# Performance work log

Measured on AMD Instinct MI355X. Metric: run time of the kernel, lower is better.

The kernel has to match this reference:

```python
import jax, jax.numpy as jnp
import numpy as np

N_NODES = 50000


def _gcn_conv(h, W, b, src, dst, dinv):
    # PyG GCNConv: linear transform, then symmetric-normalized sum aggregation
    h = h @ W  # (N, d_out)
    norm = dinv[src] * dinv[dst]  # (E,)
    msg = h[src] * norm[:, None]  # (E, d_out)
    agg = jax.ops.segment_sum(msg, dst, num_segments=N_NODES)
    return agg + b


def setup_inputs() -> dict:
    key = jax.random.key(0)
    ks = jax.random.split(key, 9)
    in_dim, h1, h2, out_dim = 512, 512, 512, 256
    x = jax.random.normal(ks[0], (N_NODES, in_dim), dtype=jnp.float32)
    edge_index = jax.random.randint(ks[1], (2, 800000), 0, N_NODES, dtype=jnp.int64)

    def glorot(k, shape):
        lim = float(np.sqrt(6.0 / (shape[0] + shape[1])))
        return jax.random.uniform(k, shape, jnp.float32, -lim, lim)

    return {
        "x": x,
        "edge_index": edge_index,
        "W1": glorot(ks[2], (in_dim, h1)),
        "b1": jnp.zeros((h1,), jnp.float32),
        "W2": glorot(ks[3], (h1, h2)),
        "b2": jnp.zeros((h2,), jnp.float32),
        "Wout": glorot(ks[4], (h2, out_dim)),
        "bout": jnp.zeros((out_dim,), jnp.float32),
    }


def reference(x, edge_index, W1, b1, W2, b2, Wout, bout):
    # add self-loops (GCNConv default)
    loop = jnp.arange(N_NODES, dtype=edge_index.dtype)
    src = jnp.concatenate([edge_index[0], loop])
    dst = jnp.concatenate([edge_index[1], loop])
    # degree on A + I (target side), deg^{-1/2}
    deg = jax.ops.segment_sum(jnp.ones_like(dst, dtype=x.dtype), dst, num_segments=N_NODES)
    dinv = jnp.where(deg > 0, jax.lax.rsqrt(deg), 0.0)

    h = jax.nn.relu(_gcn_conv(x, W1, b1, src, dst, dinv))
    h = jax.nn.relu(_gcn_conv(h, W2, b2, src, dst, dinv))
    return h @ Wout + bout
```

## Files before the change

kernel.cpp:

```cpp
#include <hip/hip_runtime.h>

#define NN 50000
#define MP 50048
#define DD 512
#define EE 800000
#define NSCAN 196
#define SCB 3321
#define CNTB 3125
#define WTB 2560
#define CVB 25024
#define CSRTOT (EE + NN + 3 * NN + 64)

typedef unsigned short u16;
typedef __attribute__((ext_vector_type(4))) float f32x4;
typedef __attribute__((ext_vector_type(8))) __bf16 bf16x8;
typedef __attribute__((ext_vector_type(8))) short s16x8;
typedef __attribute__((ext_vector_type(4))) short s16x4;

typedef __attribute__((address_space(1))) const void GVoid;
typedef __attribute__((address_space(3))) void LVoid;

__device__ __forceinline__ u16 f2bf(float f) {
  union { float f; unsigned u; } x; x.f = f;
  unsigned r = x.u + 0x7fffu + ((x.u >> 16) & 1u);
  return (u16)(r >> 16);
}
__device__ __forceinline__ float bf2f(u16 b) {
  union { unsigned u; float f; } x; x.u = ((unsigned)b) << 16;
  return x.f;
}


__global__ __launch_bounds__(256) void prep_k(const int* __restrict__ dst, int* __restrict__ cnt,
                                              const float* __restrict__ W1, u16* __restrict__ W1T,
                                              const float* __restrict__ W2, u16* __restrict__ W2T,
                                              const float* __restrict__ Wo, u16* __restrict__ WoT,
                                              const float* __restrict__ x, u16* __restrict__ xb) {
  const int b = (int)blockIdx.x, t = threadIdx.x;
  if (b < CNTB) {
    int e = b * 256 + t;
    atomicAdd(&cnt[dst[e]], 1);
    return;
  }
  if (b < CNTB + WTB) {
    int b0 = b - CNTB;
    const float* W; u16* WT; int idx, k, n;
    if (b0 < 1024)      { W = W1; WT = W1T; idx = b0 * 256 + t;          k = idx >> 9; n = idx & 511; WT[n * 512 + k] = f2bf(W[idx]); }
    else if (b0 < 2048) { W = W2; WT = W2T; idx = (b0 - 1024) * 256 + t; k = idx >> 9; n = idx & 511; WT[n * 512 + k] = f2bf(W[idx]); }
    else                { W = Wo; WT = WoT; idx = (b0 - 2048) * 256 + t; k = idx >> 8; n = idx & 255; WT[n * 512 + k] = f2bf(W[idx]); }
    return;
  }
  size_t i = ((size_t)(b - CNTB - WTB) * 256 + t) * 4;
  if (i >= (size_t)MP * DD) return;
  s16x4 v;
  if (i < (size_t)NN * DD) {
    f32x4 f = *(const f32x4*)(x + i);
    v = (s16x4){ (short)f2bf(f.x), (short)f2bf(f.y), (short)f2bf(f.z), (short)f2bf(f.w) };
  } else {
    v = (s16x4){ 0, 0, 0, 0 };
  }
  *(s16x4*)(xb + i) = v;
}


__global__ __launch_bounds__(256) void scan1_k(const int* __restrict__ cnt, int* __restrict__ bsum) {
  __shared__ int s[256];
  const int t = threadIdx.x;
  const int i = blockIdx.x * 256 + t;
  s[t] = (i < NN) ? ((cnt[i] + 1 + 3) & ~3) : 0;
  __syncthreads();
  for (int off = 128; off > 0; off >>= 1) {
    if (t < off) s[t] += s[t + off];
    __syncthreads();
  }
  if (t == 0) bsum[blockIdx.x] = s[0];
}

__global__ __launch_bounds__(256) void scan2_k(const int* __restrict__ bsum, int* __restrict__ boff) {
  __shared__ int s[256];
  const int t = threadIdx.x;
  const int v = (t < NSCAN) ? bsum[t] : 0;
  s[t] = v;
  __syncthreads();
  for (int off = 1; off < 256; off <<= 1) {
    int a = s[t];
    int b = (t >= off) ? s[t - off] : 0;
    __syncthreads();
    s[t] = a + b;
    __syncthreads();
  }
  if (t < NSCAN) boff[t] = s[t] - v;
}

__global__ __launch_bounds__(256) void scan3_k(const int* __restrict__ cnt, const int* __restrict__ boff,
                                               int* __restrict__ rowp, int* __restrict__ cursor,
                                               float* __restrict__ dinv) {
  __shared__ int s[256];
  const int t = threadIdx.x;
  const int i = blockIdx.x * 256 + t;
  const int v = (i < NN) ? (cnt[i] + 1) : 0;
  const int pv = (v + 3) & ~3;
  s[t] = pv;
  __syncthreads();
  for (int off = 1; off < 256; off <<= 1) {
    int a = s[t];
    int b = (t >= off) ? s[t - off] : 0;
    __syncthreads();
    s[t] = a + b;
    __syncthreads();
  }
  const int excl = s[t] - pv + boff[blockIdx.x];
  if (i < NN) {
    rowp[i] = excl; cursor[i] = excl;
    dinv[i] = rsqrtf((float)v);
  }
  if (i == NN - 1) rowp[NN] = excl + pv;
}


__global__ __launch_bounds__(256) void scatter_k(const int* __restrict__ src, const int* __restrict__ dst,
                                                 const float* __restrict__ dinv, int* __restrict__ cursor,
                                                 int2* __restrict__ csr) {
  int e = (int)blockIdx.x * 256 + threadIdx.x;
  if (e < EE) {
    int d = dst[e], sn = src[e];
    int pos = atomicAdd(&cursor[d], 1);
    csr[pos] = make_int2(sn << 10, __float_as_int(dinv[sn] * dinv[d]));
  } else if (e < EE + NN) {
    int i = e - EE;
    int pos = atomicAdd(&cursor[i], 1);
    float di = dinv[i];
    csr[pos] = make_int2(i << 10, __float_as_int(di * di));
  }
}


template<int OUT_BF16>
__global__ __launch_bounds__(256) void gemm_k(const u16* __restrict__ A, const u16* __restrict__ BT,
                                              void* __restrict__ Cv, const float* __restrict__ bias,
                                              int M, int N) {
  const int nwg = (int)gridDim.x;
  const int id = (int)blockIdx.x;
  const int xcd = id & 7;
  const int idx = id >> 3;
  const int q = nwg >> 3, r = nwg & 7;
  const int tile = (xcd < r ? xcd * (q + 1) : r * (q + 1) + (xcd - r) * q) + idx;
  const int ntn = N >> 7;
  const int bm = tile / ntn;
  const int bn = tile % ntn;

  __shared__ u16 As[2][128 * 32];
  __shared__ u16 Bs[2][128 * 32];
  const int t = threadIdx.x;
  const int lane = t & 63;
  const int wc = (t >> 6) & 1;
  const int wr = (t >> 7) & 1;
  f32x4 acc[4][4] = {};
  const int r0 = t >> 2;
  const int kc = (t & 3) * 8;
  const u16* Ab = A + (size_t)bm * 128 * DD + (size_t)r0 * DD + kc;
  const u16* Bb = BT + (size_t)bn * 128 * DD + (size_t)r0 * DD + kc;

  auto stage = [&](int buf, int kt) {
    __builtin_amdgcn_global_load_lds((GVoid*)(Ab + kt),           (LVoid*)(&As[buf][t * 8]),        16, 0, 0);
    __builtin_amdgcn_global_load_lds((GVoid*)(Ab + 64 * DD + kt), (LVoid*)(&As[buf][2048 + t * 8]), 16, 0, 0);
    __builtin_amdgcn_global_load_lds((GVoid*)(Bb + kt),           (LVoid*)(&Bs[buf][t * 8]),        16, 0, 0);
    __builtin_amdgcn_global_load_lds((GVoid*)(Bb + 64 * DD + kt), (LVoid*)(&Bs[buf][2048 + t * 8]), 16, 0, 0);
  };

  stage(0, 0);
  __syncthreads();

  #pragma unroll 2
  for (int step = 0; step < 16; ++step) {
    const int cur = step & 1;
    if (step < 15) stage(cur ^ 1, (step + 1) * 32);
    bf16x8 af[4], bv[4];
    #pragma unroll
    for (int m = 0; m < 4; ++m)
      af[m] = *(const bf16x8*)&As[cur][(wr * 64 + m * 16 + (lane & 15)) * 32 + (lane >> 4) * 8];
    #pragma unroll
    for (int n = 0; n < 4; ++n)
      bv[n] = *(const bf16x8*)&Bs[cur][(wc * 64 + n * 16 + (lane & 15)) * 32 + (lane >> 4) * 8];
    #pragma unroll
    for (int m = 0; m < 4; ++m) {
      #pragma unroll
      for (int n = 0; n < 4; ++n)
        acc[m][n] = __builtin_amdgcn_mfma_f32_16x16x32_bf16(af[m], bv[n], acc[m][n], 0, 0, 0);
    }
    __syncthreads();
  }

  const int rb = bm * 128 + wr * 64 + ((lane >> 4) * 4);
  const int cb = bn * 128 + wc * 64 + (lane & 15);
  #pragma unroll
  for (int m = 0; m < 4; ++m) {
    #pragma unroll
    for (int rr = 0; rr < 4; ++rr) {
      const int row = rb + m * 16 + rr;
      if (row < M) {
        #pragma unroll
        for (int n = 0; n < 4; ++n) {
          const int col = cb + n * 16;
          float v = acc[m][n][rr];
          if (bias) v += bias[col];
          if (OUT_BF16) ((u16*)Cv)[(size_t)row * N + col] = f2bf(v);
          else          ((float*)Cv)[(size_t)row * N + col] = v;
        }
      }
    }
  }
}


__global__ __launch_bounds__(256) void aggregate_k(const u16* __restrict__ H, const int* __restrict__ rowp,
                                                   const int2* __restrict__ csr,
                                                   const float* __restrict__ bias,
                                                   u16* __restrict__ out) {
  const int slice = (int)blockIdx.x & 7;
  const int grp = (int)blockIdx.x >> 3;
  const int wid = threadIdx.x >> 6;
  const int lane = threadIdx.x & 63;
  const int g = lane >> 3;
  const int l = lane & 7;
  const int node = grp * 32 + wid * 8 + g;
  if (node >= NN) return;
  const int d0 = slice * 64 + l * 8;
  const int beg = rowp[node];
  const int rounds = (rowp[node + 1] - beg) >> 2;
  const char* Hb = (const char*)H + (size_t)d0 * 2;
  const int4* cp = (const int4*)(csr + beg);
  float a0 = 0.f, a1 = 0.f, a2 = 0.f, a3 = 0.f, a4 = 0.f, a5 = 0.f, a6 = 0.f, a7 = 0.f;

  int4 c01 = cp[0], c23 = cp[1];
  for (int b = 0; b < rounds; ++b) {
    const s16x8 v0 = *(const s16x8*)(Hb + c01.x);
    const s16x8 v1 = *(const s16x8*)(Hb + c01.z);
    const s16x8 v2 = *(const s16x8*)(Hb + c23.x);
    const s16x8 v3 = *(const s16x8*)(Hb + c23.z);
    const int4 n01 = cp[2 * b + 2], n23 = cp[2 * b + 3];
    const float w0 = __int_as_float(c01.y), w1 = __int_as_float(c01.w);
    const float w2 = __int_as_float(c23.y), w3 = __int_as_float(c23.w);
    a0 += bf2f((u16)v0[0]) * w0 + bf2f((u16)v1[0]) * w1 + bf2f((u16)v2[0]) * w2 + bf2f((u16)v3[0]) * w3;
    a1 += bf2f((u16)v0[1]) * w0 + bf2f((u16)v1[1]) * w1 + bf2f((u16)v2[1]) * w2 + bf2f((u16)v3[1]) * w3;
    a2 += bf2f((u16)v0[2]) * w0 + bf2f((u16)v1[2]) * w1 + bf2f((u16)v2[2]) * w2 + bf2f((u16)v3[2]) * w3;
    a3 += bf2f((u16)v0[3]) * w0 + bf2f((u16)v1[3]) * w1 + bf2f((u16)v2[3]) * w2 + bf2f((u16)v3[3]) * w3;
    a4 += bf2f((u16)v0[4]) * w0 + bf2f((u16)v1[4]) * w1 + bf2f((u16)v2[4]) * w2 + bf2f((u16)v3[4]) * w3;
    a5 += bf2f((u16)v0[5]) * w0 + bf2f((u16)v1[5]) * w1 + bf2f((u16)v2[5]) * w2 + bf2f((u16)v3[5]) * w3;
    a6 += bf2f((u16)v0[6]) * w0 + bf2f((u16)v1[6]) * w1 + bf2f((u16)v2[6]) * w2 + bf2f((u16)v3[6]) * w3;
    a7 += bf2f((u16)v0[7]) * w0 + bf2f((u16)v1[7]) * w1 + bf2f((u16)v2[7]) * w2 + bf2f((u16)v3[7]) * w3;
    c01 = n01; c23 = n23;
  }

  s16x8 o;
  o[0] = (short)f2bf(fmaxf(a0 + bias[d0 + 0], 0.f));
  o[1] = (short)f2bf(fmaxf(a1 + bias[d0 + 1], 0.f));
  o[2] = (short)f2bf(fmaxf(a2 + bias[d0 + 2], 0.f));
  o[3] = (short)f2bf(fmaxf(a3 + bias[d0 + 3], 0.f));
  o[4] = (short)f2bf(fmaxf(a4 + bias[d0 + 4], 0.f));
  o[5] = (short)f2bf(fmaxf(a5 + bias[d0 + 5], 0.f));
  o[6] = (short)f2bf(fmaxf(a6 + bias[d0 + 6], 0.f));
  o[7] = (short)f2bf(fmaxf(a7 + bias[d0 + 7], 0.f));
  *(s16x8*)(out + (size_t)node * DD + d0) = o;
}


extern "C" void kernel_launch(void* const* d_in, const int* in_sizes, int n_in,
                              void* d_out, int out_size, void* d_ws, size_t ws_size,
                              hipStream_t stream) {
  const float* x    = (const float*)d_in[0];
  const int*   ei   = (const int*)d_in[1];
  const float* W1   = (const float*)d_in[2];
  const float* b1   = (const float*)d_in[3];
  const float* W2   = (const float*)d_in[4];
  const float* b2   = (const float*)d_in[5];
  const float* Wout = (const float*)d_in[6];
  const float* bout = (const float*)d_in[7];
  float* out = (float*)d_out;
  (void)in_sizes; (void)n_in; (void)out_size; (void)ws_size;

  char* ws = (char*)d_ws;
  size_t off = 0;
  auto alloc = [&](size_t bytes) -> char* {
    char* p = ws + off;
    off = (off + bytes + 255) & ~(size_t)255;
    return p;
  };
  u16*   xb   = (u16*)alloc((size_t)MP * DD * 2);
  u16*   H    = (u16*)alloc((size_t)NN * DD * 2);
  u16*   W1T  = (u16*)alloc(512 * 512 * 2);
  u16*   W2T  = (u16*)alloc(512 * 512 * 2);
  u16*   WoT  = (u16*)alloc(256 * 512 * 2);
  int*   cnt  = (int*)alloc(NN * 4);
  float* dinv = (float*)alloc(NN * 4);
  int*   rowp = (int*)alloc((NN + 1) * 4);
  int*   cur  = (int*)alloc(NN * 4);
  int2*  csr  = (int2*)alloc((size_t)CSRTOT * 8);
  int*   bsum = (int*)alloc(NSCAN * 4);
  int*   boff = (int*)alloc(NSCAN * 4);

  const int* srcp = ei;
  const int* dstp = ei + EE;

  hipMemsetAsync(cnt, 0, NN * 4, stream);
  hipMemsetAsync(csr, 0, (size_t)CSRTOT * 8, stream);

  prep_k<<<CNTB + WTB + CVB, 256, 0, stream>>>(dstp, cnt, W1, W1T, W2, W2T, Wout, WoT, x, xb);
  scan1_k<<<NSCAN, 256, 0, stream>>>(cnt, bsum);
  scan2_k<<<1, 256, 0, stream>>>(bsum, boff);
  scan3_k<<<NSCAN, 256, 0, stream>>>(cnt, boff, rowp, cur, dinv);
  scatter_k<<<SCB, 256, 0, stream>>>(srcp, dstp, dinv, cur, csr);

  const int agg_grid = ((NN + 31) / 32) * 8;

  gemm_k<1><<<(MP / 128) * (512 / 128), 256, 0, stream>>>(xb, W1T, (void*)H, nullptr, NN, 512);
  aggregate_k<<<agg_grid, 256, 0, stream>>>(H, rowp, csr, b1, xb);
  gemm_k<1><<<(MP / 128) * (512 / 128), 256, 0, stream>>>(xb, W2T, (void*)H, nullptr, NN, 512);
  aggregate_k<<<agg_grid, 256, 0, stream>>>(H, rowp, csr, b2, xb);
  gemm_k<0><<<(MP / 128) * (256 / 128), 256, 0, stream>>>(xb, WoT, (void*)out, bout, NN, 256);
}
```

Before: 440.0 us.

## Use 256x128 GEMM tiles, fuse weight/x conversion into scatter, nontemporal CSR loads

The GEMM tile becomes 256x128 with 512 threads, so each block reuses the B tile across twice as many rows and the grid is halved. Padding is raised to a multiple of 256 to match. The weight transpose and x-to-bf16 conversion move out of the counting kernel and into the scatter kernel launch, leaving a lean atomic count kernel. The aggregation kernel uses nontemporal loads for CSR entries and nontemporal stores for its output to reduce cache pollution. The larger tile uses more LDS and registers per block, which may lower occupancy.

```diff
diff --git a/kernel.cpp b/kernel.cpp
--- a/kernel.cpp
+++ b/kernel.cpp
@@ -1,14 +1,14 @@
 #include <hip/hip_runtime.h>
 
 #define NN 50000
-#define MP 50048
+#define MP 50176
 #define DD 512
 #define EE 800000
 #define NSCAN 196
 #define SCB 3321
 #define CNTB 3125
 #define WTB 2560
-#define CVB 25024
+#define CVB 25088
 #define CSRTOT (EE + NN + 3 * NN + 64)
 
 typedef unsigned short u16;
@@ -16,6 +16,7 @@
 typedef __attribute__((ext_vector_type(8))) __bf16 bf16x8;
 typedef __attribute__((ext_vector_type(8))) short s16x8;
 typedef __attribute__((ext_vector_type(4))) short s16x4;
+typedef __attribute__((ext_vector_type(4))) int i32x4;
 
 typedef __attribute__((address_space(1))) const void GVoid;
 typedef __attribute__((address_space(3))) void LVoid;
@@ -31,35 +32,9 @@
 }
 
 
-__global__ __launch_bounds__(256) void prep_k(const int* __restrict__ dst, int* __restrict__ cnt,
-                                              const float* __restrict__ W1, u16* __restrict__ W1T,
-                                              const float* __restrict__ W2, u16* __restrict__ W2T,
-                                              const float* __restrict__ Wo, u16* __restrict__ WoT,
-                                              const float* __restrict__ x, u16* __restrict__ xb) {
-  const int b = (int)blockIdx.x, t = threadIdx.x;
-  if (b < CNTB) {
-    int e = b * 256 + t;
-    atomicAdd(&cnt[dst[e]], 1);
-    return;
-  }
-  if (b < CNTB + WTB) {
-    int b0 = b - CNTB;
-    const float* W; u16* WT; int idx, k, n;
-    if (b0 < 1024)      { W = W1; WT = W1T; idx = b0 * 256 + t;          k = idx >> 9; n = idx & 511; WT[n * 512 + k] = f2bf(W[idx]); }
-    else if (b0 < 2048) { W = W2; WT = W2T; idx = (b0 - 1024) * 256 + t; k = idx >> 9; n = idx & 511; WT[n * 512 + k] = f2bf(W[idx]); }
-    else                { W = Wo; WT = WoT; idx = (b0 - 2048) * 256 + t; k = idx >> 8; n = idx & 255; WT[n * 512 + k] = f2bf(W[idx]); }
-    return;
-  }
-  size_t i = ((size_t)(b - CNTB - WTB) * 256 + t) * 4;
-  if (i >= (size_t)MP * DD) return;
-  s16x4 v;
-  if (i < (size_t)NN * DD) {
-    f32x4 f = *(const f32x4*)(x + i);
-    v = (s16x4){ (short)f2bf(f.x), (short)f2bf(f.y), (short)f2bf(f.z), (short)f2bf(f.w) };
-  } else {
-    v = (s16x4){ 0, 0, 0, 0 };
-  }
-  *(s16x4*)(xb + i) = v;
+__global__ __launch_bounds__(256) void count_k(const int* __restrict__ dst, int* __restrict__ cnt) {
+  int e = (int)blockIdx.x * 256 + threadIdx.x;
+  atomicAdd(&cnt[dst[e]], 1);
 }
 
 
@@ -118,54 +93,80 @@
 }
 
 
-__global__ __launch_bounds__(256) void scatter_k(const int* __restrict__ src, const int* __restrict__ dst,
+__global__ __launch_bounds__(256) void scatgat_k(const int* __restrict__ src, const int* __restrict__ dst,
                                                  const float* __restrict__ dinv, int* __restrict__ cursor,
-                                                 int2* __restrict__ csr) {
-  int e = (int)blockIdx.x * 256 + threadIdx.x;
-  if (e < EE) {
-    int d = dst[e], sn = src[e];
-    int pos = atomicAdd(&cursor[d], 1);
-    csr[pos] = make_int2(sn << 10, __float_as_int(dinv[sn] * dinv[d]));
-  } else if (e < EE + NN) {
-    int i = e - EE;
-    int pos = atomicAdd(&cursor[i], 1);
-    float di = dinv[i];
-    csr[pos] = make_int2(i << 10, __float_as_int(di * di));
-  }
+                                                 int2* __restrict__ csr,
+                                                 const float* __restrict__ W1, u16* __restrict__ W1T,
+                                                 const float* __restrict__ W2, u16* __restrict__ W2T,
+                                                 const float* __restrict__ Wo, u16* __restrict__ WoT,
+                                                 const float* __restrict__ x, u16* __restrict__ xb) {
+  const int b = (int)blockIdx.x, t = threadIdx.x;
+  if (b < SCB) {
+    int e = b * 256 + t;
+    if (e < EE) {
+      int d = dst[e], sn = src[e];
+      int pos = atomicAdd(&cursor[d], 1);
+      csr[pos] = make_int2(sn << 10, __float_as_int(dinv[sn] * dinv[d]));
+    } else if (e < EE + NN) {
+      int i = e - EE;
+      int pos = atomicAdd(&cursor[i], 1);
+      float di = dinv[i];
+      csr[pos] = make_int2(i << 10, __float_as_int(di * di));
+    }
+    return;
+  }
+  if (b < SCB + WTB) {
+    int b0 = b - SCB;
+    int idx, k, n;
+    if (b0 < 1024)      { idx = b0 * 256 + t;          k = idx >> 9; n = idx & 511; W1T[n * 512 + k] = f2bf(W1[idx]); }
+    else if (b0 < 2048) { idx = (b0 - 1024) * 256 + t; k = idx >> 9; n = idx & 511; W2T[n * 512 + k] = f2bf(W2[idx]); }
+    else                { idx = (b0 - 2048) * 256 + t; k = idx >> 8; n = idx & 255; WoT[n * 512 + k] = f2bf(Wo[idx]); }
+    return;
+  }
+  size_t i = ((size_t)(b - SCB - WTB) * 256 + t) * 4;
+  if (i >= (size_t)MP * DD) return;
+  s16x4 v;
+  if (i < (size_t)NN * DD) {
+    f32x4 f = *(const f32x4*)(x + i);
+    v = (s16x4){ (short)f2bf(f.x), (short)f2bf(f.y), (short)f2bf(f.z), (short)f2bf(f.w) };
+  } else {
+    v = (s16x4){ 0, 0, 0, 0 };
+  }
+  *(s16x4*)(xb + i) = v;
 }
 
 
 template<int OUT_BF16>
-__global__ __launch_bounds__(256) void gemm_k(const u16* __restrict__ A, const u16* __restrict__ BT,
-                                              void* __restrict__ Cv, const float* __restrict__ bias,
-                                              int M, int N) {
+__global__ __launch_bounds__(512) void gemm256_k(const u16* __restrict__ A, const u16* __restrict__ BT,
+                                                 void* __restrict__ Cv, const float* __restrict__ bias,
+                                                 int M, int N) {
   const int nwg = (int)gridDim.x;
   const int id = (int)blockIdx.x;
   const int xcd = id & 7;
   const int idx = id >> 3;
-  const int q = nwg >> 3, r = nwg & 7;
-  const int tile = (xcd < r ? xcd * (q + 1) : r * (q + 1) + (xcd - r) * q) + idx;
+  const int q = nwg >> 3;
+  const int tile = xcd * q + idx;
   const int ntn = N >> 7;
   const int bm = tile / ntn;
   const int bn = tile % ntn;
 
-  __shared__ u16 As[2][128 * 32];
+  __shared__ u16 As[2][256 * 32];
   __shared__ u16 Bs[2][128 * 32];
   const int t = threadIdx.x;
   const int lane = t & 63;
-  const int wc = (t >> 6) & 1;
-  const int wr = (t >> 7) & 1;
+  const int wid = t >> 6;
+  const int wm = wid >> 1;
+  const int wn = wid & 1;
   f32x4 acc[4][4] = {};
   const int r0 = t >> 2;
   const int kc = (t & 3) * 8;
-  const u16* Ab = A + (size_t)bm * 128 * DD + (size_t)r0 * DD + kc;
+  const u16* Ab = A + (size_t)bm * 256 * DD + (size_t)r0 * DD + kc;
   const u16* Bb = BT + (size_t)bn * 128 * DD + (size_t)r0 * DD + kc;
 
   auto stage = [&](int buf, int kt) {
-    __builtin_amdgcn_global_load_lds((GVoid*)(Ab + kt),           (LVoid*)(&As[buf][t * 8]),        16, 0, 0);
-    __builtin_amdgcn_global_load_lds((GVoid*)(Ab + 64 * DD + kt), (LVoid*)(&As[buf][2048 + t * 8]), 16, 0, 0);
-    __builtin_amdgcn_global_load_lds((GVoid*)(Bb + kt),           (LVoid*)(&Bs[buf][t * 8]),        16, 0, 0);
-    __builtin_amdgcn_global_load_lds((GVoid*)(Bb + 64 * DD + kt), (LVoid*)(&Bs[buf][2048 + t * 8]), 16, 0, 0);
+    __builtin_amdgcn_global_load_lds((GVoid*)(Ab + kt),            (LVoid*)(&As[buf][t * 8]),        16, 0, 0);
+    __builtin_amdgcn_global_load_lds((GVoid*)(Ab + 128 * DD + kt), (LVoid*)(&As[buf][4096 + t * 8]), 16, 0, 0);
+    __builtin_amdgcn_global_load_lds((GVoid*)(Bb + kt),            (LVoid*)(&Bs[buf][t * 8]),        16, 0, 0);
   };
 
   stage(0, 0);
@@ -178,10 +179,10 @@
     bf16x8 af[4], bv[4];
     #pragma unroll
     for (int m = 0; m < 4; ++m)
-      af[m] = *(const bf16x8*)&As[cur][(wr * 64 + m * 16 + (lane & 15)) * 32 + (lane >> 4) * 8];
+      af[m] = *(const bf16x8*)&As[cur][(wm * 64 + m * 16 + (lane & 15)) * 32 + (lane >> 4) * 8];
     #pragma unroll
     for (int n = 0; n < 4; ++n)
-      bv[n] = *(const bf16x8*)&Bs[cur][(wc * 64 + n * 16 + (lane & 15)) * 32 + (lane >> 4) * 8];
+      bv[n] = *(const bf16x8*)&Bs[cur][(wn * 64 + n * 16 + (lane & 15)) * 32 + (lane >> 4) * 8];
     #pragma unroll
     for (int m = 0; m < 4; ++m) {
       #pragma unroll
@@ -191,8 +192,8 @@
     __syncthreads();
   }
 
-  const int rb = bm * 128 + wr * 64 + ((lane >> 4) * 4);
-  const int cb = bn * 128 + wc * 64 + (lane & 15);
+  const int rb = bm * 256 + wm * 64 + ((lane >> 4) * 4);
+  const int cb = bn * 128 + wn * 64 + (lane & 15);
   #pragma unroll
   for (int m = 0; m < 4; ++m) {
     #pragma unroll
@@ -202,10 +203,8 @@
         #pragma unroll
         for (int n = 0; n < 4; ++n) {
           const int col = cb + n * 16;
-          float v = acc[m][n][rr];
-          if (bias) v += bias[col];
-          if (OUT_BF16) ((u16*)Cv)[(size_t)row * N + col] = f2bf(v);
-          else          ((float*)Cv)[(size_t)row * N + col] = v;
+          if (OUT_BF16) ((u16*)Cv)[(size_t)row * N + col] = f2bf(acc[m][n][rr]);
+          else          ((float*)Cv)[(size_t)row * N + col] = acc[m][n][rr] + bias[col];
         }
       }
     }
@@ -229,16 +228,18 @@
   const int beg = rowp[node];
   const int rounds = (rowp[node + 1] - beg) >> 2;
   const char* Hb = (const char*)H + (size_t)d0 * 2;
-  const int4* cp = (const int4*)(csr + beg);
+  const i32x4* cp = (const i32x4*)(csr + beg);
   float a0 = 0.f, a1 = 0.f, a2 = 0.f, a3 = 0.f, a4 = 0.f, a5 = 0.f, a6 = 0.f, a7 = 0.f;
 
-  int4 c01 = cp[0], c23 = cp[1];
+  i32x4 c01 = __builtin_nontemporal_load(cp);
+  i32x4 c23 = __builtin_nontemporal_load(cp + 1);
   for (int b = 0; b < rounds; ++b) {
     const s16x8 v0 = *(const s16x8*)(Hb + c01.x);
     const s16x8 v1 = *(const s16x8*)(Hb + c01.z);
     const s16x8 v2 = *(const s16x8*)(Hb + c23.x);
     const s16x8 v3 = *(const s16x8*)(Hb + c23.z);
-    const int4 n01 = cp[2 * b + 2], n23 = cp[2 * b + 3];
+    const i32x4 n01 = __builtin_nontemporal_load(cp + 2 * b + 2);
+    const i32x4 n23 = __builtin_nontemporal_load(cp + 2 * b + 3);
     const float w0 = __int_as_float(c01.y), w1 = __int_as_float(c01.w);
     const float w2 = __int_as_float(c23.y), w3 = __int_as_float(c23.w);
     a0 += bf2f((u16)v0[0]) * w0 + bf2f((u16)v1[0]) * w1 + bf2f((u16)v2[0]) * w2 + bf2f((u16)v3[0]) * w3;
@@ -261,7 +262,7 @@
   o[5] = (short)f2bf(fmaxf(a5 + bias[d0 + 5], 0.f));
   o[6] = (short)f2bf(fmaxf(a6 + bias[d0 + 6], 0.f));
   o[7] = (short)f2bf(fmaxf(a7 + bias[d0 + 7], 0.f));
-  *(s16x8*)(out + (size_t)node * DD + d0) = o;
+  __builtin_nontemporal_store(o, (s16x8*)(out + (size_t)node * DD + d0));
 }
 
 
@@ -302,20 +303,21 @@
   const int* srcp = ei;
   const int* dstp = ei + EE;
 
-  hipMemsetAsync(cnt, 0, NN * 4, stream);
-  hipMemsetAsync(csr, 0, (size_t)CSRTOT * 8, stream);
-
-  prep_k<<<CNTB + WTB + CVB, 256, 0, stream>>>(dstp, cnt, W1, W1T, W2, W2T, Wout, WoT, x, xb);
+  (void)hipMemsetAsync(cnt, 0, NN * 4, stream);
+  (void)hipMemsetAsync(csr, 0, (size_t)CSRTOT * 8, stream);
+
+  count_k<<<CNTB, 256, 0, stream>>>(dstp, cnt);
   scan1_k<<<NSCAN, 256, 0, stream>>>(cnt, bsum);
   scan2_k<<<1, 256, 0, stream>>>(bsum, boff);
   scan3_k<<<NSCAN, 256, 0, stream>>>(cnt, boff, rowp, cur, dinv);
-  scatter_k<<<SCB, 256, 0, stream>>>(srcp, dstp, dinv, cur, csr);
+  scatgat_k<<<SCB + WTB + CVB, 256, 0, stream>>>(srcp, dstp, dinv, cur, csr,
+                                                 W1, W1T, W2, W2T, Wout, WoT, x, xb);
 
   const int agg_grid = ((NN + 31) / 32) * 8;
 
-  gemm_k<1><<<(MP / 128) * (512 / 128), 256, 0, stream>>>(xb, W1T, (void*)H, nullptr, NN, 512);
+  gemm256_k<1><<<(MP / 256) * (512 / 128), 512, 0, stream>>>(xb, W1T, (void*)H, nullptr, NN, 512);
   aggregate_k<<<agg_grid, 256, 0, stream>>>(H, rowp, csr, b1, xb);
-  gemm_k<1><<<(MP / 128) * (512 / 128), 256, 0, stream>>>(xb, W2T, (void*)H, nullptr, NN, 512);
+  gemm256_k<1><<<(MP / 256) * (512 / 128), 512, 0, stream>>>(xb, W2T, (void*)H, nullptr, NN, 512);
   aggregate_k<<<agg_grid, 256, 0, stream>>>(H, rowp, csr, b2, xb);
-  gemm_k<0><<<(MP / 128) * (256 / 128), 256, 0, stream>>>(xb, WoT, (void*)out, bout, NN, 256);
-}
+  gemm256_k<0><<<(MP / 256) * (256 / 128), 512, 0, stream>>>(xb, WoT, (void*)out, bout, NN, 256);
+}
```

Measured after the change: 521.9 us. 18.6% more time.
